# Performance work log

Measured on AMD Instinct MI355X. Metric: run time of the kernel, lower is better.

Reference implementation:

```python
import jax, jax.numpy as jnp
import numpy as np

K = 10
ALPHA = 0.1


def setup_inputs() -> dict:
    key = jax.random.key(0)
    k1, k2, k3, k4 = jax.random.split(key, 4)
    N, E, D_IN, D_OUT = 100000, 3200000, 128, 64
    x = jax.random.normal(k1, (N, D_IN), dtype=jnp.float32)
    edge_index = jax.random.randint(k2, (2, E), 0, N, dtype=jnp.int64)
    W = jax.random.normal(k3, (D_IN, D_OUT), dtype=jnp.float32) / np.sqrt(D_IN)
    b = jax.random.normal(k4, (D_OUT,), dtype=jnp.float32) * 0.01
    return {"x": x, "edge_index": edge_index, "W": W, "b": b}


def reference(x, edge_index, W, b):
    N = x.shape[0]
    # gcn_norm with self-loops (PyG default for APPNP when edge_weight is None)
    loop = jnp.arange(N, dtype=edge_index.dtype)
    src = jnp.concatenate([edge_index[0], loop])  # [E+N]
    dst = jnp.concatenate([edge_index[1], loop])
    ew = jnp.ones(src.shape[0], dtype=x.dtype)
    deg = jax.ops.segment_sum(ew, dst, num_segments=N)  # in-degree incl. self-loop
    dinv = jnp.where(deg > 0, jax.lax.rsqrt(deg), 0.0)
    norm = dinv[src] * ew * dinv[dst]  # [E+N]

    # K-step personalized PageRank propagation: h = (1-alpha) * A_hat h + alpha * x
    h = x
    for _ in range(K):
        msg = h[src] * norm[:, None]  # gather + scale, [E+N, D]
        agg = jax.ops.segment_sum(msg, dst, num_segments=N)  # scatter-add
        h = (1.0 - ALPHA) * agg + ALPHA * x

    return h @ W + b
```

## Files before the change

### kernel.cpp

```cpp
#include <hip/hip_runtime.h>
#include <hip/hip_fp16.h>
#include <math.h>


#define BSH 8


__global__ void zero_i32(int* __restrict__ p, int n) {
    int i = blockIdx.x * blockDim.x + threadIdx.x;
    if (i < n) p[i] = 0;
}

__global__ void zero_dummy(__half2* __restrict__ b0, __half2* __restrict__ b1,
                           __half2* __restrict__ b2, int N) {
    int t = threadIdx.x;
    if (t >= 96) return;
    __half2* b = (t < 32) ? b0 : (t < 64) ? b1 : b2;
    b[(size_t)N * 32 + (t & 31)] = __floats2half2_rn(0.f, 0.f);
}


__global__ void __launch_bounds__(256) bucket_hist_k(const int* __restrict__ dst, int E,
                                                     int* __restrict__ bktcnt) {
    __shared__ int hist[400];
    int t = threadIdx.x;
    for (int i = t; i < 400; i += 256) hist[i] = 0;
    __syncthreads();
    int e0 = blockIdx.x * 4096 + t;
#pragma unroll
    for (int i = 0; i < 16; ++i) {
        int e = e0 + i * 256;
        if (e < E) atomicAdd(&hist[dst[e] >> BSH], 1);
    }
    __syncthreads();
    for (int b = t; b < 400; b += 256) {
        int c = hist[b];
        if (c > 0) atomicAdd(&bktcnt[b], c);
    }
}


__global__ void bucket_scan_k(const int* __restrict__ bktcnt, int nb, int E,
                              int* __restrict__ bktbase, int* __restrict__ bktcur) {
    __shared__ int s[256];
    int t = threadIdx.x;
    int C = (nb + 255) / 256;
    int b0 = t * C;
    int loc[8]; int sum = 0;
    for (int i = 0; i < C; ++i) {
        int v = (b0 + i < nb) ? bktcnt[b0 + i] : 0;
        loc[i] = sum; sum += v;
    }
    s[t] = sum; __syncthreads();
    for (int off = 1; off < 256; off <<= 1) {
        int v = (t >= off) ? s[t - off] : 0;
        __syncthreads();
        s[t] += v;
        __syncthreads();
    }
    int excl = s[t] - sum;
    for (int i = 0; i < C; ++i)
        if (b0 + i < nb) {
            int e0 = excl + loc[i];
            bktbase[b0 + i] = e0;
            bktcur[(b0 + i) * 16] = e0;
        }
    if (t == 0) bktbase[nb] = E;
}


__global__ void __launch_bounds__(256) binsort_k(const int* __restrict__ src,
                                                 const int* __restrict__ dst, int E,
                                                 int* __restrict__ bktcur,
                                                 unsigned* __restrict__ binned) {
    __shared__ int hist[400], gbase[400], lcur[400];
    int t = threadIdx.x;
    for (int i = t; i < 400; i += 256) { hist[i] = 0; lcur[i] = 0; }
    __syncthreads();

    int e0 = blockIdx.x * 4096 + t;
    unsigned rec[16]; int bk[16];
#pragma unroll
    for (int i = 0; i < 16; ++i) {
        int e = e0 + i * 256;
        if (e < E) {
            int s = src[e], d = dst[e];
            bk[i]  = d >> BSH;
            rec[i] = ((unsigned)s << BSH) | (unsigned)(d & 255);
            atomicAdd(&hist[bk[i]], 1);
        } else bk[i] = -1;
    }
    __syncthreads();
    for (int b = t; b < 400; b += 256) {
        int c = hist[b];
        if (c > 0) gbase[b] = atomicAdd(&bktcur[b * 16], c);
    }
    __syncthreads();
#pragma unroll
    for (int i = 0; i < 16; ++i) {
        if (bk[i] >= 0) {
            int loc = atomicAdd(&lcur[bk[i]], 1);
            binned[gbase[bk[i]] + loc] = rec[i];
        }
    }
}


__global__ void __launch_bounds__(256) fill2_k(const unsigned* __restrict__ binned,
                                               const int* __restrict__ bktbase,
                                               int N, int E, int NB,
                                               int* __restrict__ rowptr,
                                               float* __restrict__ dinv,
                                               int* __restrict__ col) {
    __shared__ int cnt[256], excl[256], lcur[256];
    int b = blockIdx.x, t = threadIdx.x;
    int beg = bktbase[b], end = bktbase[b + 1];
    cnt[t] = 0;
    __syncthreads();
    for (int i = beg + t; i < end; i += 256)
        atomicAdd(&cnt[binned[i] & 255u], 1);
    __syncthreads();
    int v = cnt[t];
    excl[t] = v;
    __syncthreads();
    for (int off = 1; off < 256; off <<= 1) {
        int u = (t >= off) ? excl[t - off] : 0;
        __syncthreads();
        excl[t] += u;
        __syncthreads();
    }
    int ex = excl[t] - v;
    lcur[t] = ex;
    int d = (b << BSH) + t;
    if (d < N) {
        rowptr[d] = beg + ex;
        dinv[d] = rsqrtf((float)(v + 1));
    }
    if (b == NB - 1 && t == 0) rowptr[N] = E;
    __syncthreads();
    for (int i = beg + t; i < end; i += 256) {
        unsigned r = binned[i];
        int loc = atomicAdd(&lcur[r & 255u], 1);
        col[beg + loc] = (int)(r >> BSH);
    }
}


__global__ void __launch_bounds__(256) gemm_k(const float* __restrict__ x,
                                              const float* __restrict__ W,
                                              const float* __restrict__ dinv,
                                              __half2* __restrict__ g0f,
                                              __half2* __restrict__ g0h, int N) {
    __shared__ float Ws[128 * 64];
    __shared__ float xs[128 * 133];
    int t = threadIdx.x;
    for (int i = t; i < 128 * 64; i += 256) Ws[i] = W[i];
    int n0 = blockIdx.x * 128;
    for (int f = t; f < 128 * 32; f += 256) {
        int r = f >> 5, c4 = f & 31;
        int n = n0 + r;
        float4 v = (n < N) ? ((const float4*)x)[(size_t)n * 32 + c4]
                           : make_float4(0.f, 0.f, 0.f, 0.f);
        float* dp = &xs[r * 133 + c4 * 4];
        dp[0] = v.x; dp[1] = v.y; dp[2] = v.z; dp[3] = v.w;
    }
    __syncthreads();
    int tr = t & 15, tc = t >> 4;
    int j0 = tr * 4, r0 = tc * 8;
    float acc[8][4] = {};
#pragma unroll 4
    for (int k = 0; k < 128; ++k) {
        float4 wv = *(const float4*)&Ws[k * 64 + j0];
#pragma unroll
        for (int i = 0; i < 8; ++i) {
            float xv = xs[(r0 + i) * 133 + k];
            acc[i][0] += xv * wv.x; acc[i][1] += xv * wv.y;
            acc[i][2] += xv * wv.z; acc[i][3] += xv * wv.w;
        }
    }
    int h0 = j0 >> 1;
#pragma unroll
    for (int i = 0; i < 8; ++i) {
        int n = n0 + r0 + i;
        if (n < N) {
            float dn = dinv[n];
            __half2* gf = &g0f[(size_t)n * 32 + h0];
            gf[0] = __floats2half2_rn(acc[i][0], acc[i][1]);
            gf[1] = __floats2half2_rn(acc[i][2], acc[i][3]);
            __half2* gp = &g0h[(size_t)n * 32 + h0];
            gp[0] = __floats2half2_rn(acc[i][0] * dn, acc[i][1] * dn);
            gp[1] = __floats2half2_rn(acc[i][2] * dn, acc[i][3] * dn);
        }
    }
}


__global__ void __launch_bounds__(256) prop_k(const __half2* __restrict__ gin,
                                              const __half2* __restrict__ g0f,
                                              __half2* __restrict__ gout,
                                              float* __restrict__ outf,
                                              const int* __restrict__ rowptr,
                                              const int* __restrict__ cols,
                                              const float* __restrict__ dinv,
                                              const float* __restrict__ bias,
                                              int N, int final_step) {
    int gw = (blockIdx.x * blockDim.x + threadIdx.x) >> 6;
    int lane = threadIdx.x & 63;
    if (gw >= N) return;
    int lh   = lane & 31;
    int pair = lane >> 5;

    int beg = rowptr[gw], end = rowptr[gw + 1];
    int deg = end - beg;

    float di   = dinv[gw];
    float2 gi  = __half22float2(gin[(size_t)gw * 32 + lh]);
    float2 g0v = __half22float2(g0f[(size_t)gw * 32 + lh]);

    float ax = 0.f, ay = 0.f;

    for (int base = 0; base < deg; base += 64) {
        int m = deg - base; if (m > 64) m = 64;
        int idx = beg + base + (lane < m ? lane : 0);
        int ci = cols[idx];
        int j = 0;
        for (; j + 7 < m; j += 8) {
            float2 f[4];
#pragma unroll
            for (int u = 0; u < 4; ++u) {
                int ce = __builtin_amdgcn_readlane(ci, j + 2 * u);
                int co = __builtin_amdgcn_readlane(ci, j + 2 * u + 1);
                int c  = pair ? co : ce;
                f[u] = __half22float2(gin[(size_t)c * 32 + lh]);
            }
#pragma unroll
            for (int u = 0; u < 4; ++u) { ax += f[u].x; ay += f[u].y; }
        }
        if (j < m) {
            float2 f[4];
#pragma unroll
            for (int u = 0; u < 4; ++u) {
                int e  = j + 2 * u;
                int ce = __builtin_amdgcn_readlane(ci, e < 63 ? e : 63);
                int co = __builtin_amdgcn_readlane(ci, e + 1 < 63 ? e + 1 : 63);
                int c  = pair ? co : ce;
                if (e + pair >= m) c = N;
                f[u] = __half22float2(gin[(size_t)c * 32 + lh]);
            }
#pragma unroll
            for (int u = 0; u < 4; ++u) { ax += f[u].x; ay += f[u].y; }
        }
    }

    ax += __shfl(ax, lane ^ 32, 64);
    ay += __shfl(ay, lane ^ 32, 64);

    if (pair == 0) {
        float rx = 0.9f * di * (ax + gi.x) + 0.1f * g0v.x;
        float ry = 0.9f * di * (ay + gi.y) + 0.1f * g0v.y;
        if (final_step) {
            float2 bv = ((const float2*)bias)[lh];
            ((float2*)outf)[(size_t)gw * 32 + lh] = make_float2(rx + bv.x, ry + bv.y);
        } else {
            gout[(size_t)gw * 32 + lh] = __floats2half2_rn(di * rx, di * ry);
        }
    }
}


extern "C" void kernel_launch(void* const* d_in, const int* in_sizes, int n_in,
                              void* d_out, int out_size, void* d_ws, size_t ws_size,
                              hipStream_t stream) {
    const float* x  = (const float*)d_in[0];
    const int*   ei = (const int*)d_in[1];
    const float* W  = (const float*)d_in[2];
    const float* b  = (const float*)d_in[3];
    float* out = (float*)d_out;

    const int N = in_sizes[0] / 128;
    const int E = in_sizes[1] / 2;
    const int* src = ei;
    const int* dst = ei + E;
    const int NB = (N + 255) >> BSH;

    char* w = (char*)d_ws;
    size_t off = 0;
    auto alloc = [&](size_t bytes) -> void* {
        void* p = w + off;
        off += (bytes + 255) & ~(size_t)255;
        return p;
    };
    const size_t fp16buf = (size_t)(N + 1) * 32 * sizeof(__half2);
    __half2*  g0h    = (__half2*) alloc(fp16buf);
    __half2*  bufA   = (__half2*) alloc(fp16buf);
    __half2*  bufB   = (__half2*) alloc(fp16buf);
    __half2*  g0f    = (__half2*) alloc(fp16buf);
    int*      cols   = (int*)     alloc((size_t)E * 4);
    unsigned* binned = (unsigned*)alloc((size_t)E * 4);
    int*      rowptr = (int*)     alloc((size_t)(N + 1) * 4);
    int*      bktcnt = (int*)     alloc((size_t)NB * 4);
    int*      bktbase= (int*)     alloc((size_t)(NB + 1) * 4);
    int*      bktcur = (int*)     alloc((size_t)NB * 16 * 4);
    float*    dinvv  = (float*)   alloc((size_t)N * 4);

    const int nblkB = (E + 4095) / 4096;

    zero_i32<<<(NB + 255) / 256, 256, 0, stream>>>(bktcnt, NB);
    bucket_hist_k<<<nblkB, 256, 0, stream>>>(dst, E, bktcnt);
    zero_dummy<<<1, 96, 0, stream>>>(g0h, bufA, bufB, N);
    bucket_scan_k<<<1, 256, 0, stream>>>(bktcnt, NB, E, bktbase, bktcur);
    binsort_k<<<nblkB, 256, 0, stream>>>(src, dst, E, bktcur, binned);
    fill2_k<<<NB, 256, 0, stream>>>(binned, bktbase, N, E, NB, rowptr, dinvv, cols);

    gemm_k<<<(N + 127) / 128, 256, 0, stream>>>(x, W, dinvv, g0f, g0h, N);

    const int nblkP = (N * 64 + 255) / 256;
    const __half2* gin = g0h;
    __half2* pp[2] = {bufA, bufB};
    for (int k = 0; k < 10; ++k) {
        const bool fin = (k == 9);
        __half2* gout = pp[k & 1];
        prop_k<<<nblkP, 256, 0, stream>>>(gin, g0f, gout, out, rowptr, cols,
                                          dinvv, b, N, fin ? 1 : 0);
        gin = gout;
    }
}
```

Baseline: 872.8 us.

## Gather neighbor rows with 16-byte loads across 8 sub-groups per wavefront

The propagation kernel now splits each 64-lane wavefront into 8 sub-groups of 8 lanes. Each lane loads 16 bytes (8 fp16 values) of a neighbor row, so 8 edges are gathered in parallel instead of 2, and a butterfly shuffle reduction combines the partial sums. This is meant to raise memory-level parallelism and cut instruction count per gathered byte, at the cost of an 8-register accumulator and more shuffle work at the end. The GEMM is also reshaped to 64-row tiles that read W straight from global memory instead of staging it in LDS, lowering shared-memory use so more blocks fit per CU.

Result: faster. 760.1 us (-12.9%).

```diff
diff --git a/kernel.cpp b/kernel.cpp
--- a/kernel.cpp
+++ b/kernel.cpp
@@ -151,12 +151,10 @@
                                               const float* __restrict__ dinv,
                                               __half2* __restrict__ g0f,
                                               __half2* __restrict__ g0h, int N) {
-    __shared__ float Ws[128 * 64];
-    __shared__ float xs[128 * 133];
-    int t = threadIdx.x;
-    for (int i = t; i < 128 * 64; i += 256) Ws[i] = W[i];
-    int n0 = blockIdx.x * 128;
-    for (int f = t; f < 128 * 32; f += 256) {
+    __shared__ float xs[64 * 133];
+    int t = threadIdx.x;
+    int n0 = blockIdx.x * 64;
+    for (int f = t; f < 64 * 32; f += 256) {
         int r = f >> 5, c4 = f & 31;
         int n = n0 + r;
         float4 v = (n < N) ? ((const float4*)x)[(size_t)n * 32 + c4]
@@ -166,13 +164,14 @@
     }
     __syncthreads();
     int tr = t & 15, tc = t >> 4;
-    int j0 = tr * 4, r0 = tc * 8;
-    float acc[8][4] = {};
-#pragma unroll 4
+    int j0 = tr * 4, r0 = tc * 4;
+    const float4* W4 = (const float4*)W;
+    float acc[4][4] = {};
+#pragma unroll 8
     for (int k = 0; k < 128; ++k) {
-        float4 wv = *(const float4*)&Ws[k * 64 + j0];
-#pragma unroll
-        for (int i = 0; i < 8; ++i) {
+        float4 wv = W4[k * 16 + tr];
+#pragma unroll
+        for (int i = 0; i < 4; ++i) {
             float xv = xs[(r0 + i) * 133 + k];
             acc[i][0] += xv * wv.x; acc[i][1] += xv * wv.y;
             acc[i][2] += xv * wv.z; acc[i][3] += xv * wv.w;
@@ -180,7 +179,7 @@
     }
     int h0 = j0 >> 1;
 #pragma unroll
-    for (int i = 0; i < 8; ++i) {
+    for (int i = 0; i < 4; ++i) {
         int n = n0 + r0 + i;
         if (n < N) {
             float dn = dinv[n];
@@ -207,62 +206,70 @@
     int gw = (blockIdx.x * blockDim.x + threadIdx.x) >> 6;
     int lane = threadIdx.x & 63;
     if (gw >= N) return;
-    int lh   = lane & 31;
-    int pair = lane >> 5;
+    int sub = lane >> 3;
+    int q   = lane & 7;
 
     int beg = rowptr[gw], end = rowptr[gw + 1];
     int deg = end - beg;
 
-    float di   = dinv[gw];
-    float2 gi  = __half22float2(gin[(size_t)gw * 32 + lh]);
-    float2 g0v = __half22float2(g0f[(size_t)gw * 32 + lh]);
-
-    float ax = 0.f, ay = 0.f;
-
-    for (int base = 0; base < deg; base += 64) {
-        int m = deg - base; if (m > 64) m = 64;
-        int idx = beg + base + (lane < m ? lane : 0);
-        int ci = cols[idx];
-        int j = 0;
-        for (; j + 7 < m; j += 8) {
-            float2 f[4];
+    const char* gb = (const char*)gin;
+
+    float di    = dinv[gw];
+    float4 giv  = *(const float4*)(gb + (size_t)gw * 128 + q * 16);
+    float4 g0v4 = *(const float4*)((const char*)g0f + (size_t)gw * 128 + q * 16);
+
+    float a[8] = {};
+
+    for (int base = 0; base < deg; base += 32) {
+        int m = deg - base; if (m > 32) m = 32;
+        int l32 = lane & 31;
+        int ci = cols[beg + base + (l32 < m ? l32 : 0)];
+#pragma unroll
+        for (int i = 0; i < 4; ++i) {
+            int e = i * 8 + sub;
+            int c = __shfl(ci, e, 64);
+            if (base + e >= deg) c = N;
+            float4 v = *(const float4*)(gb + (size_t)c * 128 + q * 16);
+            const __half2* h2 = (const __half2*)&v;
 #pragma unroll
             for (int u = 0; u < 4; ++u) {
-                int ce = __builtin_amdgcn_readlane(ci, j + 2 * u);
-                int co = __builtin_amdgcn_readlane(ci, j + 2 * u + 1);
-                int c  = pair ? co : ce;
-                f[u] = __half22float2(gin[(size_t)c * 32 + lh]);
+                float2 f = __half22float2(h2[u]);
+                a[2 * u]     += f.x;
+                a[2 * u + 1] += f.y;
             }
-#pragma unroll
-            for (int u = 0; u < 4; ++u) { ax += f[u].x; ay += f[u].y; }
-        }
-        if (j < m) {
-            float2 f[4];
-#pragma unroll
-            for (int u = 0; u < 4; ++u) {
-                int e  = j + 2 * u;
-                int ce = __builtin_amdgcn_readlane(ci, e < 63 ? e : 63);
-                int co = __builtin_amdgcn_readlane(ci, e + 1 < 63 ? e + 1 : 63);
-                int c  = pair ? co : ce;
-                if (e + pair >= m) c = N;
-                f[u] = __half22float2(gin[(size_t)c * 32 + lh]);
-            }
-#pragma unroll
-            for (int u = 0; u < 4; ++u) { ax += f[u].x; ay += f[u].y; }
-        }
-    }
-
-    ax += __shfl(ax, lane ^ 32, 64);
-    ay += __shfl(ay, lane ^ 32, 64);
-
-    if (pair == 0) {
-        float rx = 0.9f * di * (ax + gi.x) + 0.1f * g0v.x;
-        float ry = 0.9f * di * (ay + gi.y) + 0.1f * g0v.y;
+        }
+    }
+
+#pragma unroll
+    for (int off = 8; off < 64; off <<= 1) {
+#pragma unroll
+        for (int u = 0; u < 8; ++u) a[u] += __shfl_xor(a[u], off, 64);
+    }
+
+    if (sub == 0) {
+        const __half2* gih = (const __half2*)&giv;
+        const __half2* g0h2 = (const __half2*)&g0v4;
+        float r[8];
+#pragma unroll
+        for (int u = 0; u < 4; ++u) {
+            float2 gi = __half22float2(gih[u]);
+            float2 g0 = __half22float2(g0h2[u]);
+            r[2 * u]     = 0.9f * di * (a[2 * u]     + gi.x) + 0.1f * g0.x;
+            r[2 * u + 1] = 0.9f * di * (a[2 * u + 1] + gi.y) + 0.1f * g0.y;
+        }
         if (final_step) {
-            float2 bv = ((const float2*)bias)[lh];
-            ((float2*)outf)[(size_t)gw * 32 + lh] = make_float2(rx + bv.x, ry + bv.y);
+            float4 b0 = ((const float4*)bias)[2 * q];
+            float4 b1 = ((const float4*)bias)[2 * q + 1];
+            float4 o0 = make_float4(r[0] + b0.x, r[1] + b0.y, r[2] + b0.z, r[3] + b0.w);
+            float4 o1 = make_float4(r[4] + b1.x, r[5] + b1.y, r[6] + b1.z, r[7] + b1.w);
+            float4* op = (float4*)(outf + (size_t)gw * 64 + q * 8);
+            op[0] = o0; op[1] = o1;
         } else {
-            gout[(size_t)gw * 32 + lh] = __floats2half2_rn(di * rx, di * ry);
+            __half2 o[4];
+#pragma unroll
+            for (int u = 0; u < 4; ++u)
+                o[u] = __floats2half2_rn(di * r[2 * u], di * r[2 * u + 1]);
+            *(float4*)((char*)gout + (size_t)gw * 128 + q * 16) = *(float4*)o;
         }
     }
 }
@@ -312,7 +319,7 @@
     binsort_k<<<nblkB, 256, 0, stream>>>(src, dst, E, bktcur, binned);
     fill2_k<<<NB, 256, 0, stream>>>(binned, bktbase, N, E, NB, rowptr, dinvv, cols);
 
-    gemm_k<<<(N + 127) / 128, 256, 0, stream>>>(x, W, dinvv, g0f, g0h, N);
+    gemm_k<<<(N + 63) / 64, 256, 0, stream>>>(x, W, dinvv, g0f, g0h, N);
 
     const int nblkP = (N * 64 + 255) / 256;
     const __half2* gin = g0h;
```
